# Optimization experiments

Measured on AMD Instinct MI355X. Metric: run time of the kernel, lower is better.

## Reference

```python
import jax, jax.numpy as jnp
import numpy as np

NUM_HEADS = 12

def setup_inputs() -> dict:
    key = jax.random.key(0)
    ks = jax.random.split(key, 6)
    B, N, C = 8, 1024, 768
    H = W = 32
    rel_sp_dim = 2 * H - 1  # 63
    head_dim = C // NUM_HEADS  # 64
    s = 0.02
    return {
        "x": jax.random.normal(ks[0], (B, N, C), dtype=jnp.float32),
        "qkv_w": jax.random.normal(ks[1], (3 * C, C), dtype=jnp.float32) * s,
        "rel_pos_h": jax.random.normal(ks[2], (rel_sp_dim, head_dim), dtype=jnp.float32) * s,
        "rel_pos_w": jax.random.normal(ks[3], (rel_sp_dim, head_dim), dtype=jnp.float32) * s,
        "proj_w": jax.random.normal(ks[4], (C, C), dtype=jnp.float32) * s,
        "proj_b": jax.random.normal(ks[5], (C,), dtype=jnp.float32) * s,
        "H": H,
        "W": W,
    }

def reference(x, qkv_w, rel_pos_h, rel_pos_w, proj_w, proj_b, H, W):
    B, N, C = x.shape
    nh = NUM_HEADS
    hd = C // nh
    scale = hd ** -0.5

    # QKV projection (no bias)
    qkv = (x @ qkv_w.T).reshape(B, N, 3, nh, hd)
    qkv = jnp.transpose(qkv, (2, 0, 3, 1, 4))  # [3, B, nh, N, hd]
    q, k, v = qkv[0] * scale, qkv[1], qkv[2]

    attn = jnp.einsum('bhqd,bhkd->bhqk', q, k)  # [B, nh, N, N]

    # relative position bias (q_shape == k_shape, so ratios are 1)
    dist_h = jnp.arange(H)[:, None] - jnp.arange(H)[None, :] + (H - 1)
    dist_w = jnp.arange(W)[:, None] - jnp.arange(W)[None, :] + (W - 1)
    Rh = rel_pos_h[dist_h]  # [H, H, hd]
    Rw = rel_pos_w[dist_w]  # [W, W, hd]

    r_q = q.reshape(B, nh, H, W, hd)
    rel_h = jnp.einsum('byhwc,hkc->byhwk', r_q, Rh)  # [B, nh, H, W, H]
    rel_w = jnp.einsum('byhwc,wkc->byhwk', r_q, Rw)  # [B, nh, H, W, W]

    attn = attn.reshape(B, nh, H, W, H, W)
    attn = attn + rel_h[:, :, :, :, :, None] + rel_w[:, :, :, :, None, :]
    attn = attn.reshape(B, nh, N, N)

    attn = jax.nn.softmax(attn, axis=-1)
    out = jnp.einsum('bhqk,bhkd->bhqd', attn, v)  # [B, nh, N, hd]
    out = jnp.transpose(out, (0, 2, 1, 3)).reshape(B, N, C)
    return out @ proj_w.T + proj_b
```

## Files before the change

kernel.cpp:

```cpp
#include <hip/hip_runtime.h>

#define DEVI __device__ __forceinline__

typedef float f32x4 __attribute__((ext_vector_type(4)));
typedef float f32x16 __attribute__((ext_vector_type(16)));
typedef short bf16x8 __attribute__((ext_vector_type(8)));
typedef unsigned int uint2v __attribute__((ext_vector_type(2)));

DEVI unsigned short f2bf(float f) {
  union { float f; unsigned int u; } v; v.f = f;
  unsigned int u = v.u;
  u += 0x7fffu + ((u >> 16) & 1u);
  return (unsigned short)(u >> 16);
}
DEVI float bf2f(unsigned short h) {
  union { unsigned int u; float f; } v; v.u = ((unsigned int)h) << 16;
  return v.f;
}

DEVI void gld_lds16(const void* g, void* l) {
  __builtin_amdgcn_global_load_lds(
      (const __attribute__((address_space(1))) void*)g,
      (__attribute__((address_space(3))) void*)l, 16, 0, 0);
}

DEVI unsigned int cvt_pk_bf16(float lo, float hi) {
  unsigned int r;
  asm("v_cvt_pk_bf16_f32 %0, %1, %2" : "=v"(r) : "v"(lo), "v"(hi));
  return r;
}

DEVI float exp2_raw(float x) {
  float r;
  asm("v_exp_f32 %0, %1" : "=v"(r) : "v"(x));
  return r;
}

#define MFMA16(a, b, c) __builtin_amdgcn_mfma_f32_16x16x32_bf16((a), (b), (c), 0, 0, 0)
#define MFMA32(a, b, c) __builtin_amdgcn_mfma_f32_32x32x16_bf16((a), (b), (c), 0, 0, 0)

#define QSCALE 0.18033688011112042f

__global__ void __launch_bounds__(256) convert3_kernel(
    const float* __restrict__ x, const float* __restrict__ qkv_w,
    const float* __restrict__ proj_w,
    unsigned short* __restrict__ xb, unsigned short* __restrict__ wqkv,
    unsigned short* __restrict__ wproj) {
  const int i = blockIdx.x * 256 + threadIdx.x;
  const float* src; unsigned short* dst; int off;
  if (i < 1572864)      { src = x;      dst = xb;    off = i; }
  else if (i < 2015232) { src = qkv_w;  dst = wqkv;  off = i - 1572864; }
  else                  { src = proj_w; dst = wproj; off = i - 2015232; }
  float4 v = ((const float4*)src)[off];
  ushort4 o;
  o.x = f2bf(v.x); o.y = f2bf(v.y); o.z = f2bf(v.z); o.w = f2bf(v.w);
  ((ushort4*)dst)[off] = o;
}

template <int MODE>
__global__ void __launch_bounds__(256) gemm_nt(
    const unsigned short* __restrict__ A,
    const unsigned short* __restrict__ Bw,
    unsigned short* __restrict__ oq,
    unsigned short* __restrict__ okk,
    unsigned short* __restrict__ ovt,
    float* __restrict__ of,
    const float* __restrict__ bias) {
  constexpr int K = 768;
  constexpr int NT = K / 64;
  const int tid = threadIdx.x;
  const int l = tid & 63, wv = tid >> 6;
  const int wy = wv >> 1, wx = wv & 1;
  const int lg = l >> 4, lr = l & 15;
  const int m0 = blockIdx.x * 128, n0 = blockIdx.y * 128;

  __shared__ __align__(16) unsigned short As[2][128 * 64];
  __shared__ __align__(16) unsigned short Bs[2][128 * 64];

  f32x4 acc[4][4] = {};

  auto stage = [&](int buf, int k0) {
#pragma unroll
    for (int c = 0; c < 4; ++c) {
      const int row = c * 32 + wv * 8 + (l >> 3);
      const int g = l & 7;
      const int off = ((g ^ (row & 7)) * 8);
      gld_lds16(A + (size_t)(m0 + row) * K + k0 + off, &As[buf][(c * 32 + wv * 8) * 64]);
      gld_lds16(Bw + (size_t)(n0 + row) * K + k0 + off, &Bs[buf][(c * 32 + wv * 8) * 64]);
    }
  };

  stage(0, 0);

  int cur = 0;
  for (int t = 0; t < NT; ++t) {
    if (t + 1 < NT) {
      stage(cur ^ 1, (t + 1) * 64);
      asm volatile("s_waitcnt vmcnt(8)" ::: "memory");
    } else {
      asm volatile("s_waitcnt vmcnt(0)" ::: "memory");
    }
    __builtin_amdgcn_s_barrier();
    __builtin_amdgcn_sched_barrier(0);

#pragma unroll
    for (int kk = 0; kk < 2; ++kk) {
      bf16x8 af[4], bfr[4];
#pragma unroll
      for (int i = 0; i < 4; ++i) {
        const int row = wy * 64 + i * 16 + lr;
        af[i] = *(const bf16x8*)&As[cur][row * 64 + (((kk * 4 + lg) ^ (row & 7)) * 8)];
      }
#pragma unroll
      for (int j = 0; j < 4; ++j) {
        const int row = wx * 64 + j * 16 + lr;
        bfr[j] = *(const bf16x8*)&Bs[cur][row * 64 + (((kk * 4 + lg) ^ (row & 7)) * 8)];
      }
#pragma unroll
      for (int i = 0; i < 4; ++i) {
#pragma unroll
        for (int j = 0; j < 4; ++j)
          acc[i][j] = MFMA16(af[i], bfr[j], acc[i][j]);
      }
    }

    asm volatile("s_waitcnt lgkmcnt(0)" ::: "memory");
    __builtin_amdgcn_sched_barrier(0);
    __builtin_amdgcn_s_barrier();
    cur ^= 1;
  }

  if constexpr (MODE == 0) {
    const int t = n0 / 768;
    if (t < 2) {
      unsigned short* base = (t == 0) ? oq : okk;
      const float sc = (t == 0) ? QSCALE : 1.0f;
#pragma unroll
      for (int i = 0; i < 4; ++i) {
        const int m = m0 + wy * 64 + i * 16 + lg * 4;
#pragma unroll
        for (int j = 0; j < 4; ++j) {
          const int col = n0 + wx * 64 + j * 16 + lr;
          const int rem = col - t * 768;
          const int h = rem >> 6, d = rem & 63;
#pragma unroll
          for (int r = 0; r < 4; ++r) {
            const int mm = m + r;
            const int b = mm >> 10, n = mm & 1023;
            base[(((size_t)(b * 12 + h) << 10) + n) * 64 + d] = f2bf(acc[i][j][r] * sc);
          }
        }
      }
    } else {
#pragma unroll
      for (int i = 0; i < 4; ++i) {
        const int m = m0 + wy * 64 + i * 16 + lg * 4;
        const int b = m >> 10, ntok = m & 1023;
#pragma unroll
        for (int j = 0; j < 4; ++j) {
          const int col = n0 + wx * 64 + j * 16 + lr;
          const int rem = col - 1536;
          const int h = rem >> 6, d = rem & 63;
          ushort4 pk4;
          pk4.x = f2bf(acc[i][j][0]); pk4.y = f2bf(acc[i][j][1]);
          pk4.z = f2bf(acc[i][j][2]); pk4.w = f2bf(acc[i][j][3]);
          *(ushort4*)(ovt + ((size_t)(b * 12 + h) * 64 + d) * 1024 + ntok) = pk4;
        }
      }
    }
  } else {
#pragma unroll
    for (int i = 0; i < 4; ++i) {
      const int m = m0 + wy * 64 + i * 16 + lg * 4;
#pragma unroll
      for (int j = 0; j < 4; ++j) {
        const int col = n0 + wx * 64 + j * 16 + lr;
        const float bv = bias[col];
#pragma unroll
        for (int r = 0; r < 4; ++r)
          of[(size_t)(m + r) * 768 + col] = acc[i][j][r] + bv;
      }
    }
  }
}

__global__ void __launch_bounds__(256) rel_kernel(
    const unsigned short* __restrict__ Q,
    const float* __restrict__ rph,
    const float* __restrict__ rpw,
    unsigned short* __restrict__ relh_t,
    unsigned short* __restrict__ relw_t) {
  const int bh = blockIdx.y;
  const int tid = threadIdx.x;
  const int l = tid & 63, w = tid >> 6;
  const int hi = l >> 5, l31 = l & 31;
  const int yx = blockIdx.x * 4 + w;

  const unsigned short* Qb = Q + (size_t)bh * 65536;

  f32x16 acch = {};
#pragma unroll
  for (int s4 = 0; s4 < 4; ++s4) {
    const float* ar = rph + (yx + 31 - l31) * 64 + s4 * 16 + hi * 8;
    float4 fa = ((const float4*)ar)[0], fb = ((const float4*)ar)[1];
    union { unsigned int u[4]; bf16x8 v; } au;
    au.u[0] = cvt_pk_bf16(fa.x, fa.y); au.u[1] = cvt_pk_bf16(fa.z, fa.w);
    au.u[2] = cvt_pk_bf16(fb.x, fb.y); au.u[3] = cvt_pk_bf16(fb.z, fb.w);
    bf16x8 qv = *(const bf16x8*)(Qb + (size_t)(yx * 32 + l31) * 64 + s4 * 16 + hi * 8);
    acch = MFMA32(au.v, qv, acch);
  }
  {
    unsigned short* ob = relh_t + (size_t)bh * 32768 + yx * 32 + l31;
#pragma unroll
    for (int r = 0; r < 16; ++r) {
      const int kh = (r & 3) + 8 * (r >> 2) + 4 * hi;
      ob[(size_t)kh * 1024] = f2bf(acch[r]);
    }
  }

  f32x16 accw = {};
#pragma unroll
  for (int s4 = 0; s4 < 4; ++s4) {
    const float* ar = rpw + (yx + 31 - l31) * 64 + s4 * 16 + hi * 8;
    float4 fa = ((const float4*)ar)[0], fb = ((const float4*)ar)[1];
    union { unsigned int u[4]; bf16x8 v; } au;
    au.u[0] = cvt_pk_bf16(fa.x, fa.y); au.u[1] = cvt_pk_bf16(fa.z, fa.w);
    au.u[2] = cvt_pk_bf16(fb.x, fb.y); au.u[3] = cvt_pk_bf16(fb.z, fb.w);
    bf16x8 qv = *(const bf16x8*)(Qb + (size_t)(l31 * 32 + yx) * 64 + s4 * 16 + hi * 8);
    accw = MFMA32(au.v, qv, accw);
  }
  {
    unsigned short* ob = relw_t + (size_t)bh * 32768 + l31 * 32 + yx;
#pragma unroll
    for (int r = 0; r < 16; ++r) {
      const int kw = (r & 3) + 8 * (r >> 2) + 4 * hi;
      ob[(size_t)kw * 1024] = f2bf(accw[r]);
    }
  }
}

__global__ void __launch_bounds__(256, 3) attn_kernel(
    const unsigned short* __restrict__ Q,
    const unsigned short* __restrict__ Km,
    const unsigned short* __restrict__ VT,
    const unsigned short* __restrict__ relh_t,
    const unsigned short* __restrict__ relw_t,
    unsigned short* __restrict__ out) {
  const int bid = blockIdx.x;
  const int qt = bid / 96;
  const int bh = bid % 96;
  const int q0 = qt * 128;
  const int tid = threadIdx.x;
  const int l = tid & 63, w = tid >> 6;
  const int hi = l >> 5, l31 = l & 31;

  __shared__ __align__(16) unsigned short Ks[2][64 * 64];
  __shared__ __align__(16) unsigned short VTs[2][64 * 64];

  const unsigned short* Kb = Km + (size_t)bh * 65536;
  const unsigned short* Vb = VT + (size_t)bh * 65536;

  unsigned int rhpk[16];
  {
    const unsigned short* rhb = relh_t + (size_t)bh * 32768 + q0 + w * 32 + l31;
#pragma unroll
    for (int t = 0; t < 16; ++t) {
      const unsigned int lo = rhb[(size_t)(2 * t) * 1024];
      const unsigned int hi2 = rhb[(size_t)(2 * t + 1) * 1024];
      rhpk[t] = (hi2 << 16) | lo;
    }
  }

  auto stage = [&](int buf, int t) {
#pragma unroll
    for (int c = 0; c < 2; ++c) {
      const int row = c * 32 + w * 8 + (l >> 3);
      const int g = l & 7;
      const int off = (g ^ (row & 7)) * 8;
      gld_lds16(Kb + (size_t)(t * 64 + row) * 64 + off, &Ks[buf][(c * 32 + w * 8) * 64]);
      gld_lds16(Vb + (size_t)row * 1024 + t * 64 + off, &VTs[buf][(c * 32 + w * 8) * 64]);
    }
  };

  bf16x8 qf[4];
  {
    const unsigned short* qp =
        Q + (size_t)bh * 65536 + (size_t)(q0 + w * 32 + l31) * 64 + hi * 8;
#pragma unroll
    for (int s4 = 0; s4 < 4; ++s4) qf[s4] = *(const bf16x8*)(qp + s4 * 16);
  }

  f32x16 rwacc;
  bf16x8 onesA;
  {
    bf16x8 idA0, idA1, rwB0, rwB1;
    const short onebf = (short)0x3F80;
#pragma unroll
    for (int e = 0; e < 8; ++e) {
      idA0[e] = (l31 == hi * 8 + e) ? onebf : (short)0;
      idA1[e] = (l31 == 16 + hi * 8 + e) ? onebf : (short)0;
      onesA[e] = onebf;
      rwB0[e] = (short)relw_t[(size_t)bh * 32768 + (size_t)(hi * 8 + e) * 1024 +
                              q0 + w * 32 + l31];
      rwB1[e] = (short)relw_t[(size_t)bh * 32768 + (size_t)(16 + hi * 8 + e) * 1024 +
                              q0 + w * 32 + l31];
    }
    f32x16 z = {};
    rwacc = MFMA32(idA0, rwB0, z);
    rwacc = MFMA32(idA1, rwB1, rwacc);
  }

  f32x16 od0 = {}, od1 = {}, sumacc = {};
  int cur = 0;

  stage(0, 0);

#pragma unroll
  for (int t = 0; t < 16; ++t) {
    if (t < 15) {
      stage(cur ^ 1, t + 1);
      asm volatile("s_waitcnt vmcnt(4)" ::: "memory");
    } else {
      asm volatile("s_waitcnt vmcnt(0)" ::: "memory");
    }
    __builtin_amdgcn_s_barrier();
    __builtin_amdgcn_sched_barrier(0);

    f32x16 s0, s1;
    __builtin_amdgcn_s_setprio(1);
    {
      const int row0 = l31, row1 = 32 + l31;
      bf16x8 kf0 = *(const bf16x8*)&Ks[cur][row0 * 64 + ((hi ^ (row0 & 7)) * 8)];
      bf16x8 kf1 = *(const bf16x8*)&Ks[cur][row1 * 64 + ((hi ^ (row1 & 7)) * 8)];
      s0 = MFMA32(kf0, qf[0], rwacc);
      s1 = MFMA32(kf1, qf[0], rwacc);
    }
#pragma unroll
    for (int s4 = 1; s4 < 4; ++s4) {
      {
        const int row = l31;
        bf16x8 kf = *(const bf16x8*)&Ks[cur][row * 64 + (((s4 * 2 + hi) ^ (row & 7)) * 8)];
        s0 = MFMA32(kf, qf[s4], s0);
      }
      {
        const int row = 32 + l31;
        bf16x8 kf = *(const bf16x8*)&Ks[cur][row * 64 + (((s4 * 2 + hi) ^ (row & 7)) * 8)];
        s1 = MFMA32(kf, qf[s4], s1);
      }
    }
    __builtin_amdgcn_s_setprio(0);

    const float rh0 = __uint_as_float(rhpk[t] << 16);
    const float rh1 = __uint_as_float(rhpk[t] & 0xffff0000u);
#pragma unroll
    for (int r = 0; r < 16; ++r) {
      s0[r] = exp2_raw(s0[r] + rh0);
      s1[r] = exp2_raw(s1[r] + rh1);
    }

    bf16x8 pa[4];
#pragma unroll
    for (int ks = 0; ks < 4; ++ks) {
      unsigned int c0, c1, c2, c3;
      if (ks == 0) {
        c0 = cvt_pk_bf16(s0[0], s0[1]);  c1 = cvt_pk_bf16(s0[2], s0[3]);
        c2 = cvt_pk_bf16(s0[4], s0[5]);  c3 = cvt_pk_bf16(s0[6], s0[7]);
      } else if (ks == 1) {
        c0 = cvt_pk_bf16(s0[8], s0[9]);  c1 = cvt_pk_bf16(s0[10], s0[11]);
        c2 = cvt_pk_bf16(s0[12], s0[13]); c3 = cvt_pk_bf16(s0[14], s0[15]);
      } else if (ks == 2) {
        c0 = cvt_pk_bf16(s1[0], s1[1]);  c1 = cvt_pk_bf16(s1[2], s1[3]);
        c2 = cvt_pk_bf16(s1[4], s1[5]);  c3 = cvt_pk_bf16(s1[6], s1[7]);
      } else {
        c0 = cvt_pk_bf16(s1[8], s1[9]);  c1 = cvt_pk_bf16(s1[10], s1[11]);
        c2 = cvt_pk_bf16(s1[12], s1[13]); c3 = cvt_pk_bf16(s1[14], s1[15]);
      }
      uint2v x = __builtin_amdgcn_permlane32_swap(c0, c2, false, false);
      uint2v z = __builtin_amdgcn_permlane32_swap(c1, c3, false, false);
      union { unsigned int u[4]; bf16x8 v; } uu;
      uu.u[0] = x.x; uu.u[1] = z.x; uu.u[2] = x.y; uu.u[3] = z.y;
      pa[ks] = uu.v;
    }

    __builtin_amdgcn_s_setprio(1);
#pragma unroll
    for (int ks = 0; ks < 4; ++ks) {
      {
        const int row = l31;
        bf16x8 vf = *(const bf16x8*)&VTs[cur][row * 64 + (((ks * 2 + hi) ^ (row & 7)) * 8)];
        od0 = MFMA32(vf, pa[ks], od0);
      }
      {
        const int row = 32 + l31;
        bf16x8 vf = *(const bf16x8*)&VTs[cur][row * 64 + (((ks * 2 + hi) ^ (row & 7)) * 8)];
        od1 = MFMA32(vf, pa[ks], od1);
      }
      sumacc = MFMA32(onesA, pa[ks], sumacc);
    }
    __builtin_amdgcn_s_setprio(0);

    asm volatile("s_waitcnt lgkmcnt(0)" ::: "memory");
    __builtin_amdgcn_sched_barrier(0);
    __builtin_amdgcn_s_barrier();
    cur ^= 1;
  }

  const float inv = 1.f / sumacc[0];
  const int b = bh / 12, h = bh % 12;
  const int n = q0 + w * 32 + l31;
  unsigned short* ob = out + ((size_t)(b * 1024 + n)) * 768 + h * 64;
#pragma unroll
  for (int r4 = 0; r4 < 4; ++r4) {
    ushort4 p0, p1;
    p0.x = f2bf(od0[r4 * 4 + 0] * inv); p0.y = f2bf(od0[r4 * 4 + 1] * inv);
    p0.z = f2bf(od0[r4 * 4 + 2] * inv); p0.w = f2bf(od0[r4 * 4 + 3] * inv);
    p1.x = f2bf(od1[r4 * 4 + 0] * inv); p1.y = f2bf(od1[r4 * 4 + 1] * inv);
    p1.z = f2bf(od1[r4 * 4 + 2] * inv); p1.w = f2bf(od1[r4 * 4 + 3] * inv);
    *(ushort4*)(ob + 8 * r4 + 4 * hi) = p0;
    *(ushort4*)(ob + 32 + 8 * r4 + 4 * hi) = p1;
  }
}

extern "C" void kernel_launch(void* const* d_in, const int* in_sizes, int n_in,
                              void* d_out, int out_size, void* d_ws, size_t ws_size,
                              hipStream_t stream) {
  const float* x      = (const float*)d_in[0];
  const float* qkv_w  = (const float*)d_in[1];
  const float* rph    = (const float*)d_in[2];
  const float* rpw    = (const float*)d_in[3];
  const float* proj_w = (const float*)d_in[4];
  const float* proj_b = (const float*)d_in[5];
  float* out = (float*)d_out;

  char* ws = (char*)d_ws;
  unsigned short* xb     = (unsigned short*)(ws);
  unsigned short* wqkv   = (unsigned short*)(ws + 12582912);
  unsigned short* wproj  = (unsigned short*)(ws + 16121856);
  unsigned short* qb     = (unsigned short*)(ws + 17301504);
  unsigned short* kb     = (unsigned short*)(ws + 29884416);
  unsigned short* vbT    = (unsigned short*)(ws + 42467328);
  unsigned short* relh_t = (unsigned short*)(ws + 55050240);
  unsigned short* relw_t = (unsigned short*)(ws + 61341696);

  convert3_kernel<<<8448, 256, 0, stream>>>(x, qkv_w, proj_w, xb, wqkv, wproj);

  gemm_nt<0><<<dim3(64, 18), 256, 0, stream>>>(xb, wqkv, qb, kb, vbT, nullptr, nullptr);

  rel_kernel<<<dim3(8, 96), 256, 0, stream>>>(qb, rph, rpw, relh_t, relw_t);

  attn_kernel<<<768, 256, 0, stream>>>(qb, kb, vbT, relh_t, relw_t, xb);

  gemm_nt<1><<<dim3(64, 6), 256, 0, stream>>>(xb, wproj, nullptr, nullptr, nullptr, out, proj_b);
}
```

Measured before the change: 141.5 us.

## Triple-buffer K/V tiles and software-pipeline QK^T one tile ahead of PV

Grows the K and V LDS tiles from double to triple buffering, prefetches two tiles ahead, and computes the next tile's QK^T MFMAs before the current tile's exp and PV step so matrix work overlaps the transcendental work. The row-sum MFMA with a ones matrix is replaced by a scalar running sum per lane, combined across half-waves with a permlane32 swap at the end. Loads of relw and Q are also hoisted ahead of staging with an explicit vmcnt wait. The costs are more LDS per block (48KB vs 32KB), which may limit the 3-blocks-per-CU target, and extra live registers for the next score tile.

```diff
diff --git a/kernel.cpp b/kernel.cpp
--- a/kernel.cpp
+++ b/kernel.cpp
@@ -254,13 +254,14 @@
   const int l = tid & 63, w = tid >> 6;
   const int hi = l >> 5, l31 = l & 31;
 
-  __shared__ __align__(16) unsigned short Ks[2][64 * 64];
-  __shared__ __align__(16) unsigned short VTs[2][64 * 64];
+  __shared__ __align__(16) unsigned short Ks[3][64 * 64];
+  __shared__ __align__(16) unsigned short VTs[3][64 * 64];
 
   const unsigned short* Kb = Km + (size_t)bh * 65536;
   const unsigned short* Vb = VT + (size_t)bh * 65536;
 
   unsigned int rhpk[16];
+  bf16x8 rwB0, rwB1;
   {
     const unsigned short* rhb = relh_t + (size_t)bh * 32768 + q0 + w * 32 + l31;
 #pragma unroll
@@ -269,6 +270,35 @@
       const unsigned int hi2 = rhb[(size_t)(2 * t + 1) * 1024];
       rhpk[t] = (hi2 << 16) | lo;
     }
+#pragma unroll
+    for (int e = 0; e < 8; ++e) {
+      rwB0[e] = (short)relw_t[(size_t)bh * 32768 + (size_t)(hi * 8 + e) * 1024 +
+                              q0 + w * 32 + l31];
+      rwB1[e] = (short)relw_t[(size_t)bh * 32768 + (size_t)(16 + hi * 8 + e) * 1024 +
+                              q0 + w * 32 + l31];
+    }
+  }
+  bf16x8 qf[4];
+  {
+    const unsigned short* qp =
+        Q + (size_t)bh * 65536 + (size_t)(q0 + w * 32 + l31) * 64 + hi * 8;
+#pragma unroll
+    for (int s4 = 0; s4 < 4; ++s4) qf[s4] = *(const bf16x8*)(qp + s4 * 16);
+  }
+  asm volatile("s_waitcnt vmcnt(0)" ::: "memory");
+
+  f32x16 rwacc;
+  {
+    bf16x8 idA0, idA1;
+    const short onebf = (short)0x3F80;
+#pragma unroll
+    for (int e = 0; e < 8; ++e) {
+      idA0[e] = (l31 == hi * 8 + e) ? onebf : (short)0;
+      idA1[e] = (l31 == 16 + hi * 8 + e) ? onebf : (short)0;
+    }
+    f32x16 z = {};
+    rwacc = MFMA32(idA0, rwB0, z);
+    rwacc = MFMA32(idA1, rwB1, rwacc);
   }
 
   auto stage = [&](int buf, int t) {
@@ -282,80 +312,67 @@
     }
   };
 
-  bf16x8 qf[4];
-  {
-    const unsigned short* qp =
-        Q + (size_t)bh * 65536 + (size_t)(q0 + w * 32 + l31) * 64 + hi * 8;
-#pragma unroll
-    for (int s4 = 0; s4 < 4; ++s4) qf[s4] = *(const bf16x8*)(qp + s4 * 16);
-  }
-
-  f32x16 rwacc;
-  bf16x8 onesA;
-  {
-    bf16x8 idA0, idA1, rwB0, rwB1;
-    const short onebf = (short)0x3F80;
-#pragma unroll
-    for (int e = 0; e < 8; ++e) {
-      idA0[e] = (l31 == hi * 8 + e) ? onebf : (short)0;
-      idA1[e] = (l31 == 16 + hi * 8 + e) ? onebf : (short)0;
-      onesA[e] = onebf;
-      rwB0[e] = (short)relw_t[(size_t)bh * 32768 + (size_t)(hi * 8 + e) * 1024 +
-                              q0 + w * 32 + l31];
-      rwB1[e] = (short)relw_t[(size_t)bh * 32768 + (size_t)(16 + hi * 8 + e) * 1024 +
-                              q0 + w * 32 + l31];
-    }
-    f32x16 z = {};
-    rwacc = MFMA32(idA0, rwB0, z);
-    rwacc = MFMA32(idA1, rwB1, rwacc);
-  }
-
-  f32x16 od0 = {}, od1 = {}, sumacc = {};
-  int cur = 0;
-
-  stage(0, 0);
-
-#pragma unroll
-  for (int t = 0; t < 16; ++t) {
-    if (t < 15) {
-      stage(cur ^ 1, t + 1);
-      asm volatile("s_waitcnt vmcnt(4)" ::: "memory");
-    } else {
-      asm volatile("s_waitcnt vmcnt(0)" ::: "memory");
-    }
-    __builtin_amdgcn_s_barrier();
-    __builtin_amdgcn_sched_barrier(0);
-
-    f32x16 s0, s1;
-    __builtin_amdgcn_s_setprio(1);
+  auto qkt = [&](int b, f32x16& o0, f32x16& o1) {
     {
       const int row0 = l31, row1 = 32 + l31;
-      bf16x8 kf0 = *(const bf16x8*)&Ks[cur][row0 * 64 + ((hi ^ (row0 & 7)) * 8)];
-      bf16x8 kf1 = *(const bf16x8*)&Ks[cur][row1 * 64 + ((hi ^ (row1 & 7)) * 8)];
-      s0 = MFMA32(kf0, qf[0], rwacc);
-      s1 = MFMA32(kf1, qf[0], rwacc);
+      bf16x8 kf0 = *(const bf16x8*)&Ks[b][row0 * 64 + ((hi ^ (row0 & 7)) * 8)];
+      bf16x8 kf1 = *(const bf16x8*)&Ks[b][row1 * 64 + ((hi ^ (row1 & 7)) * 8)];
+      o0 = MFMA32(kf0, qf[0], rwacc);
+      o1 = MFMA32(kf1, qf[0], rwacc);
     }
 #pragma unroll
     for (int s4 = 1; s4 < 4; ++s4) {
       {
         const int row = l31;
-        bf16x8 kf = *(const bf16x8*)&Ks[cur][row * 64 + (((s4 * 2 + hi) ^ (row & 7)) * 8)];
-        s0 = MFMA32(kf, qf[s4], s0);
+        bf16x8 kf = *(const bf16x8*)&Ks[b][row * 64 + (((s4 * 2 + hi) ^ (row & 7)) * 8)];
+        o0 = MFMA32(kf, qf[s4], o0);
       }
       {
         const int row = 32 + l31;
-        bf16x8 kf = *(const bf16x8*)&Ks[cur][row * 64 + (((s4 * 2 + hi) ^ (row & 7)) * 8)];
-        s1 = MFMA32(kf, qf[s4], s1);
-      }
-    }
-    __builtin_amdgcn_s_setprio(0);
+        bf16x8 kf = *(const bf16x8*)&Ks[b][row * 64 + (((s4 * 2 + hi) ^ (row & 7)) * 8)];
+        o1 = MFMA32(kf, qf[s4], o1);
+      }
+    }
+  };
+
+  f32x16 od0 = {}, od1 = {};
+  float psum = 0.f;
+
+  stage(0, 0);
+  stage(1, 1);
+  asm volatile("s_waitcnt vmcnt(4)" ::: "memory");
+  __builtin_amdgcn_s_barrier();
+  __builtin_amdgcn_sched_barrier(0);
+  f32x16 s0, s1;
+  qkt(0, s0, s1);
+
+#pragma unroll
+  for (int t = 0; t < 16; ++t) {
+    const int last = (t == 15);
+    if (!last) {
+      if (t + 2 < 16) {
+        stage((t + 2) % 3, t + 2);
+        asm volatile("s_waitcnt vmcnt(4)" ::: "memory");
+      } else {
+        asm volatile("s_waitcnt vmcnt(0)" ::: "memory");
+      }
+      __builtin_amdgcn_s_barrier();
+      __builtin_amdgcn_sched_barrier(0);
+    }
+
+    f32x16 n0, n1;
+    if (!last) {
+      __builtin_amdgcn_s_setprio(1);
+      qkt((t + 1) % 3, n0, n1);
+      __builtin_amdgcn_s_setprio(0);
+    }
 
     const float rh0 = __uint_as_float(rhpk[t] << 16);
     const float rh1 = __uint_as_float(rhpk[t] & 0xffff0000u);
 #pragma unroll
     for (int r = 0; r < 16; ++r) {
-      s0[r] = exp2_raw(s0[r] + rh0);
-      s1[r] = exp2_raw(s1[r] + rh1);
+      s0[r] = exp2_raw(s0[r] + rh0); psum += s0[r];
+      s1[r] = exp2_raw(s1[r] + rh1); psum += s1[r];
     }
 
     bf16x8 pa[4];
@@ -387,25 +404,32 @@
     for (int ks = 0; ks < 4; ++ks) {
       {
         const int row = l31;
-        bf16x8 vf = *(const bf16x8*)&VTs[cur][row * 64 + (((ks * 2 + hi) ^ (row & 7)) * 8)];
+        bf16x8 vf = *(const bf16x8*)&VTs[t % 3][row * 64 + (((ks * 2 + hi) ^ (row & 7)) * 8)];
         od0 = MFMA32(vf, pa[ks], od0);
       }
       {
         const int row = 32 + l31;
-        bf16x8 vf = *(const bf16x8*)&VTs[cur][row * 64 + (((ks * 2 + hi) ^ (row & 7)) * 8)];
+        bf16x8 vf = *(const bf16x8*)&VTs[t % 3][row * 64 + (((ks * 2 + hi) ^ (row & 7)) * 8)];
         od1 = MFMA32(vf, pa[ks], od1);
       }
-      sumacc = MFMA32(onesA, pa[ks], sumacc);
     }
     __builtin_amdgcn_s_setprio(0);
 
-    asm volatile("s_waitcnt lgkmcnt(0)" ::: "memory");
-    __builtin_amdgcn_sched_barrier(0);
-    __builtin_amdgcn_s_barrier();
-    cur ^= 1;
-  }
-
-  const float inv = 1.f / sumacc[0];
+    if (!last) {
+      asm volatile("s_waitcnt lgkmcnt(0)" ::: "memory");
+      __builtin_amdgcn_sched_barrier(0);
+      __builtin_amdgcn_s_barrier();
+      s0 = n0; s1 = n1;
+    }
+  }
+
+  float sum;
+  {
+    uint2v sw = __builtin_amdgcn_permlane32_swap(__float_as_uint(psum),
+                                                 __float_as_uint(psum), false, false);
+    sum = __uint_as_float(sw.x) + __uint_as_float(sw.y);
+  }
+  const float inv = 1.f / sum;
   const int b = bh / 12, h = bh % 12;
   const int n = q0 + w * 32 + l31;
   unsigned short* ob = out + ((size_t)(b * 1024 + n)) * 768 + h * 64;
```

After: 405.8 us. 187% more time.
